# Performance work log

Measured on AMD Instinct MI355X. Metric: run time of the kernel, lower is better.

## Reference

```python
import jax, jax.numpy as jnp
import numpy as np

EPS = 1e-12

def _pdist(a, b):
    # a: [B,N,3], b: [B,M,3] -> [B,N,M] L2 distances (no huge [B,N,M,3] temp)
    sq = (jnp.sum(a * a, -1)[:, :, None] + jnp.sum(b * b, -1)[:, None, :]
          - 2.0 * jnp.einsum('bnd,bmd->bnm', a, b))
    return jnp.sqrt(jnp.maximum(sq, EPS))

def _loss_terms(skel_xyz, skel_radius, skel_nori, l3_xyz, shape_all):
    normal = shape_all[:, :, 3:6]
    shape_xyz = shape_all[:, :, :3]
    B, Ns, _ = skel_xyz.shape
    N = shape_xyz.shape[1]

    # --- loss_sample: 8 surface samples per sphere ---
    e = 0.57735027
    dirs = jnp.array([[e, e, e], [e, e, -e], [e, -e, e], [e, -e, -e],
                      [-e, e, e], [-e, e, -e], [-e, -e, e], [-e, -e, -e]],
                     dtype=skel_xyz.dtype)
    centers = jnp.repeat(skel_xyz, 8, axis=1)
    radii = jnp.repeat(skel_radius, 8, axis=1)
    sample_xyz = centers + radii * jnp.tile(dirs, (Ns, 1))[None]

    d_ss = _pdist(shape_xyz, sample_xyz)
    cd1 = jnp.sum(jnp.min(d_ss, axis=1)) / (Ns * 8)    # sample -> shape
    cd2 = jnp.sum(jnp.min(d_ss, axis=2)) / N           # shape -> sample
    loss_sample = cd1 + cd2

    # --- point2sphere / sphere2point ---
    d_sc = _pdist(shape_xyz, skel_xyz)                 # [B, N, Ns]
    sph = jnp.abs(d_sc - skel_radius[:, None, :, 0])
    loss_p2s = jnp.sum(jnp.min(sph, axis=2)) / N + jnp.sum(jnp.min(sph, axis=1)) / Ns

    loss_radius = -jnp.sum(skel_radius) / Ns

    # --- loss_normal: 30-NN of skel in shape, |dot(nori, shape normal)| ---
    d_ks = _pdist(skel_xyz, shape_xyz)                 # [B, Ns, N]
    idx30 = jax.lax.top_k(-d_ks, 30)[1]                # [B, Ns, 30]
    nn_nrm = jnp.take_along_axis(normal[:, None, :, :], idx30[..., None], axis=2)
    dots = jnp.einsum('bjd,bjkd->bjk', skel_nori, nn_nrm)
    loss_normal = jnp.sum(jnp.mean(jnp.abs(dots), axis=2)) / B

    # --- loss_skelenormal: points swept along nori, vs l3_xyz ---
    ks = (jnp.arange(30, dtype=skel_xyz.dtype) / 30.0)[None, :, None, None]
    combine = (skel_xyz[:, None] + skel_nori[:, None] * ks).reshape(B, 30 * Ns, 3)
    mind = jnp.min(_pdist(combine, l3_xyz), axis=2)
    loss_skn = 50.0 * jnp.sum(mind) / (B * Ns * 30)
    loss_skn = loss_skn + 500.0 * jnp.sum(jnp.var(mind, axis=1, ddof=1)) / B

    # --- loss_normaldist: exp barrier + hard penalty on |nori| ---
    nrm = jnp.sqrt(jnp.sum(skel_nori * skel_nori, -1) + EPS)
    loss_nd = jnp.sum(jnp.exp(-(nrm - 0.3)) + jnp.where(nrm < 0.25, 5.0, 0.0)) / (B * Ns)

    # --- loss_normalsmooth: 3-NN (incl. self) nori consistency ---
    idx3 = jax.lax.top_k(-_pdist(skel_xyz, skel_xyz), 3)[1]   # [B, Ns, 3]
    nn_nori = jnp.take_along_axis(skel_nori[:, None, :, :], idx3[..., None], axis=2)
    diff = skel_nori[:, :, None, :] - nn_nori
    loss_ns = jnp.sum(jnp.sqrt(jnp.sum(diff * diff, -1) + EPS)) / (B * Ns * 3)

    return loss_sample, loss_p2s, loss_radius, loss_normal, loss_skn, loss_nd, loss_ns

def setup_inputs() -> dict:
    key = jax.random.key(0)
    ks = jax.random.split(key, 9)
    B, N, Ns, M = 8, 4096, 256, 256
    return {
        'skel_xyz': jax.random.normal(ks[0], (B, Ns, 3), jnp.float32),
        'skel_radius': jax.random.uniform(ks[1], (B, Ns, 1), jnp.float32),
        'shape_cmb_features': jax.random.normal(ks[2], (B, Ns, 32), jnp.float32),
        'skel_nori': jax.random.normal(ks[3], (B, Ns, 3), jnp.float32),
        'weights': jax.random.uniform(ks[4], (B, Ns, 8), jnp.float32),
        'l3_xyz': jax.random.normal(ks[5], (B, M, 3), jnp.float32),
        'l3_normals': jax.random.normal(ks[6], (B, M, 3), jnp.float32),
        'shape_xyz': jax.random.normal(ks[7], (B, N, 6), jnp.float32),
        'A': jax.random.uniform(ks[8], (B, Ns, Ns), jnp.float32),
        'w0': 1, 'w1': 1, 'w2': 1, 'w3': 1, 'w4': 1, 'w5': 1, 'w6': 1,
    }

def reference(skel_xyz, skel_radius, shape_cmb_features, skel_nori, weights,
              l3_xyz, l3_normals, shape_xyz, A,
              w0, w1, w2, w3, w4, w5, w6):
    ls, lp, lr, ln, lskn, lnd, lns = _loss_terms(
        skel_xyz, skel_radius, skel_nori, l3_xyz, shape_xyz)
    # lap_reg=False -> loss_smooth = 0 (w3 term vanishes)
    return (w0 * ls + lp * w1 + lr * w2 + ln * w4 + lskn * w5
            + w6 * lnd + 0.1 * lns)
```

## Files before the change

kernel.cpp:

```cpp
#include <hip/hip_runtime.h>
#include <math.h>

#define EPS 1e-12f
#define EDIR 0.57735027f
#define M2E  -1.15470054f

#define NB 8
#define NS 256
#define NP 4096
#define NM 256

#define NBLK_MEGA 2048

#define OFF_SKO 0
#define OFF_C1O (OFF_SKO + 2048*4)
#define OFF_C2O (OFF_C1O + 2048)
#define OFF_P2O (OFF_C2O + 4096)
#define OFF_SKS (OFF_P2O + 4096)
#define OFF_SKQ (OFF_SKS + 960)

typedef float f4u __attribute__((ext_vector_type(4), aligned(4)));
typedef float f2u __attribute__((ext_vector_type(2), aligned(4)));

__device__ __forceinline__ unsigned umin2(unsigned a, unsigned b){ return a<b?a:b; }
__device__ __forceinline__ unsigned umax2(unsigned a, unsigned b){ return a>b?a:b; }

__device__ __forceinline__ float wave_min(float v){
#pragma unroll
  for (int o = 32; o; o >>= 1) v = fminf(v, __shfl_xor(v, o));
  return v;
}
__device__ __forceinline__ float wave_max(float v){
#pragma unroll
  for (int o = 32; o; o >>= 1) v = fmaxf(v, __shfl_xor(v, o));
  return v;
}
__device__ __forceinline__ float wave_sum(float v){
#pragma unroll
  for (int o = 32; o; o >>= 1) v += __shfl_xor(v, o);
  return v;
}
__device__ __forceinline__ unsigned wave_min_u(unsigned v){
#pragma unroll
  for (int o = 32; o; o >>= 1){ unsigned w = __shfl_xor(v, o); v = (w < v) ? w : v; }
  return v;
}
__device__ __forceinline__ unsigned wave_max_u(unsigned v){
#pragma unroll
  for (int o = 32; o; o >>= 1){ unsigned w = __shfl_xor(v, o); v = (w > v) ? w : v; }
  return v;
}
__device__ __forceinline__ unsigned long long wave_min_u64(unsigned long long v){
#pragma unroll
  for (int o = 32; o; o >>= 1){
    unsigned long long w = __shfl_xor(v, o);
    v = (w < v) ? w : v;
  }
  return v;
}

__global__ __launch_bounds__(256) void k_mega(const float* __restrict__ skel,
                                              const float* __restrict__ rad,
                                              const float* __restrict__ nori,
                                              const float* __restrict__ l3,
                                              const float* __restrict__ shape,
                                              float* __restrict__ ws){
  __shared__ float4 lsh[NM];
  int bid  = blockIdx.x;
  int tid  = threadIdx.x;
  int wid  = tid >> 6;
  int lane = tid & 63;

  if (wid == 0){
    int row = bid;
    int b = row >> 8;
    const float* sjp = skel + (size_t)row * 3;
    float cx = sjp[0], cy = sjp[1], cz = sjp[2];
    float rj = rad[row];
    float r2j = rj * rj;
    float m2re = M2E * rj;
    const float* njp = nori + (size_t)row * 3;
    float nx = njp[0], ny = njp[1], nz = njp[2];
    const float* shb = shape + (size_t)b * NP * 6;

    unsigned a0=~0u,a1=~0u,a2=~0u,a3=~0u,a4=~0u,a5=~0u;
    unsigned b0=~0u,b1=~0u,b2=~0u,b3=~0u,b4=~0u,b5=~0u;
    float dmoA = 3.4e38f, dmiA = -3.4e38f, dmoB = 3.4e38f, dmiB = -3.4e38f;
    float mn[8];
#pragma unroll
    for (int k = 0; k < 8; ++k) mn[k] = 3.4e38f;

#pragma unroll 2
    for (int s = 0; s < 32; ++s){
      int nA = s * 128 + lane;
      int nB = nA + 64;
      f4u qA = *(const f4u*)(shb + (size_t)nA * 6);
      f4u qB = *(const f4u*)(shb + (size_t)nB * 6);
      float dxA = qA.x - cx, dyA = qA.y - cy, dzA = qA.z - cz;
      float dxB = qB.x - cx, dyB = qB.y - cy, dzB = qB.z - cz;
      float dA = fmaf(dxA, dxA, fmaf(dyA, dyA, dzA * dzA));
      float dB = fmaf(dxB, dxB, fmaf(dyB, dyB, dzB * dzB));
      {
        float s1p = dxA + dyA, s2p = dxA - dyA;
        float ga = s1p + dzA, gb = s1p - dzA, gc = s2p + dzA, gd = s2p - dzA;
        mn[0] = fminf(mn[0], fmaf(m2re,  ga, dA));
        mn[1] = fminf(mn[1], fmaf(m2re,  gb, dA));
        mn[2] = fminf(mn[2], fmaf(m2re,  gc, dA));
        mn[3] = fminf(mn[3], fmaf(m2re,  gd, dA));
        mn[4] = fminf(mn[4], fmaf(m2re, -gd, dA));
        mn[5] = fminf(mn[5], fmaf(m2re, -gc, dA));
        mn[6] = fminf(mn[6], fmaf(m2re, -gb, dA));
        mn[7] = fminf(mn[7], fmaf(m2re, -ga, dA));
      }
      {
        float s1p = dxB + dyB, s2p = dxB - dyB;
        float ga = s1p + dzB, gb = s1p - dzB, gc = s2p + dzB, gd = s2p - dzB;
        mn[0] = fminf(mn[0], fmaf(m2re,  ga, dB));
        mn[1] = fminf(mn[1], fmaf(m2re,  gb, dB));
        mn[2] = fminf(mn[2], fmaf(m2re,  gc, dB));
        mn[3] = fminf(mn[3], fmaf(m2re,  gd, dB));
        mn[4] = fminf(mn[4], fmaf(m2re, -gd, dB));
        mn[5] = fminf(mn[5], fmaf(m2re, -gc, dB));
        mn[6] = fminf(mn[6], fmaf(m2re, -gb, dB));
        mn[7] = fminf(mn[7], fmaf(m2re, -ga, dB));
      }
      bool inA = dA < r2j;
      bool inB = dB < r2j;
      dmoA = fminf(dmoA, inA ? 3.4e38f : dA);
      dmiA = fmaxf(dmiA, inA ? dA : -3.4e38f);
      dmoB = fminf(dmoB, inB ? 3.4e38f : dB);
      dmiB = fmaxf(dmiB, inB ? dB : -3.4e38f);
      unsigned uA = (__float_as_uint(dA) & 0xFFFFF000u) | (unsigned)nA;
      unsigned uB = (__float_as_uint(dB) & 0xFFFFF000u) | (unsigned)nB;
      a5 = umin2(a5, uA);
      { unsigned p = umin2(a4, a5), q = umax2(a4, a5); a4 = p; a5 = q; }
      { unsigned p = umin2(a3, a4), q = umax2(a3, a4); a3 = p; a4 = q; }
      { unsigned p = umin2(a2, a3), q = umax2(a2, a3); a2 = p; a3 = q; }
      { unsigned p = umin2(a1, a2), q = umax2(a1, a2); a1 = p; a2 = q; }
      { unsigned p = umin2(a0, a1), q = umax2(a0, a1); a0 = p; a1 = q; }
      b5 = umin2(b5, uB);
      { unsigned p = umin2(b4, b5), q = umax2(b4, b5); b4 = p; b5 = q; }
      { unsigned p = umin2(b3, b4), q = umax2(b3, b4); b3 = p; b4 = q; }
      { unsigned p = umin2(b2, b3), q = umax2(b2, b3); b2 = p; b3 = q; }
      { unsigned p = umin2(b1, b2), q = umax2(b1, b2); b1 = p; b2 = q; }
      { unsigned p = umin2(b0, b1), q = umax2(b0, b1); b0 = p; b1 = q; }
    }
    {
      float v = 0.0f;
#pragma unroll
      for (int k = 0; k < 8; ++k){
        float m = wave_min(mn[k]);
        v += sqrtf(fmaxf(m + r2j, EPS));
      }
      if (lane == 0) ws[OFF_C1O + row] = v;
    }
    float dmin_out = wave_min(fminf(dmoA, dmoB));
    float dmax_in  = wave_max(fmaxf(dmiA, dmiB));
    float pmin = sqrtf(fmaxf(dmin_out, EPS)) - rj;
    float pin  = (dmax_in >= 0.0f) ? (rj - sqrtf(fmaxf(dmax_in, EPS))) : 3.4e38f;
    pmin = fminf(pmin, pin);

    unsigned lmin = umin2(a0, b0);
    unsigned lo = wave_min_u(lmin), hi = wave_max_u(lmin);
    while (lo < hi){
      unsigned mid = lo + ((hi - lo) >> 1);
      int c = __popcll(__ballot(a0 <= mid)) + __popcll(__ballot(a1 <= mid)) +
              __popcll(__ballot(a2 <= mid)) + __popcll(__ballot(a3 <= mid)) +
              __popcll(__ballot(a4 <= mid)) + __popcll(__ballot(a5 <= mid)) +
              __popcll(__ballot(b0 <= mid)) + __popcll(__ballot(b1 <= mid)) +
              __popcll(__ballot(b2 <= mid)) + __popcll(__ballot(b3 <= mid)) +
              __popcll(__ballot(b4 <= mid)) + __popcll(__ballot(b5 <= mid));
      if (c >= 30) hi = mid; else lo = mid + 1;
    }
    unsigned tau = hi;

    float dsum = 0.0f;
    {
      unsigned mm[12] = {a0,a1,a2,a3,a4,a5,b0,b1,b2,b3,b4,b5};
#pragma unroll
      for (int r = 0; r < 12; ++r){
        if (mm[r] <= tau){
          int idx = (int)(mm[r] & 0xFFFu);
          f4u qq = *(const f4u*)(shb + (size_t)idx * 6 + 2);
          dsum += fabsf(fmaf(nx, qq.y, fmaf(ny, qq.z, nz * qq.w)));
        }
      }
    }
    dsum = wave_sum(dsum);

    const float* skb = skel + (size_t)b * NS * 3;
    const float* nb  = nori + (size_t)b * NS * 3;
    unsigned u0=~0u,u1=~0u,u2=~0u; int i0=0,i1=0,i2=0;
#pragma unroll
    for (int it = 0; it < 4; ++it){
      int n2i = it * 64 + lane;
      f2u kxy = *(const f2u*)(skb + (size_t)n2i * 3);
      float kz = skb[(size_t)n2i * 3 + 2];
      float dx = kxy.x - cx, dy = kxy.y - cy, dz = kz - cz;
      unsigned u = __float_as_uint(fmaf(dx,dx,fmaf(dy,dy,dz*dz)));
      if (u < u2){ u2 = u; i2 = n2i; }
      if (u2 < u1){ unsigned t=u1;u1=u2;u2=t; int ti=i1;i1=i2;i2=ti; }
      if (u1 < u0){ unsigned t=u0;u0=u1;u1=t; int ti=i0;i0=i1;i1=ti; }
    }
    int cc = 0;
    float nssum = 0.0f;
#pragma unroll
    for (int r = 0; r < 3; ++r){
      unsigned hu = (cc==0)?u0:((cc==1)?u1:u2);
      int      hix= (cc==0)?i0:((cc==1)?i1:i2);
      unsigned long long pack = (((unsigned long long)hu) << 32) | (unsigned)hix;
      unsigned long long best = wave_min_u64(pack);
      if (pack == best) cc++;
      int idx = (int)(best & 0xffffffffull);
      if (lane == 0){
        float axn = nb[idx*3+0]-nx, ayn = nb[idx*3+1]-ny, azn = nb[idx*3+2]-nz;
        nssum += sqrtf(fmaf(axn,axn,fmaf(ayn,ayn,azn*azn)) + EPS);
      }
    }

    if (lane == 0){
      float nrm = sqrtf(nx*nx + ny*ny + nz*nz + EPS);
      float ndv = expf(0.3f - nrm) + ((nrm < 0.25f) ? 5.0f : 0.0f);
      float* sko = ws + OFF_SKO + (size_t)row * 4;
      sko[0] = pmin;
      sko[1] = dsum * (1.0f / 30.0f);
      sko[2] = nssum;
      sko[3] = ndv;
    }

  } else if (wid <= 2){
    int wv   = bid * 2 + (wid - 1);
    int row0 = wv * 8;
    int b    = row0 >> 12;
    float cx[8], cy[8], cz[8];
#pragma unroll
    for (int i = 0; i < 8; ++i){
      f4u qp = *(const f4u*)(shape + (size_t)(row0 + i) * 6);
      cx[i] = qp.x; cy[i] = qp.y; cz[i] = qp.z;
    }
    const float* skb = skel + (size_t)b * NS * 3;
    const float* rdb = rad + (size_t)b * NS;
    float mn[8], pm[8];
#pragma unroll
    for (int i = 0; i < 8; ++i){ mn[i] = 3.4e38f; pm[i] = 3.4e38f; }
#pragma unroll
    for (int it = 0; it < 4; ++it){
      int kidx = it * 64 + lane;
      f2u kxy = *(const f2u*)(skb + (size_t)kidx * 3);
      float kz = skb[(size_t)kidx * 3 + 2];
      float rr = rdb[kidx];
      float r2 = rr * rr;
      float c1 = M2E * rr;
#pragma unroll
      for (int i = 0; i < 8; ++i){
        float dx = cx[i] - kxy.x, dy = cy[i] - kxy.y, dz = cz[i] - kz;
        float q  = fmaf(dx, dx, fmaf(dy, dy, dz * dz));
        float s  = (fabsf(dx) + fabsf(dy)) + fabsf(dz);
        mn[i] = fminf(mn[i], fmaf(c1, s, q + r2));
        float d = sqrtf(fmaxf(q, EPS));
        pm[i] = fminf(pm[i], fabsf(d - rr));
      }
    }
    float cdv = 0.0f, pv = 0.0f;
#pragma unroll
    for (int i = 0; i < 8; ++i){
      float m = wave_min(mn[i]);
      cdv += sqrtf(fmaxf(m, EPS));
      pv  += wave_min(pm[i]);
    }
    if (lane == 0){
      ws[OFF_C2O + wv] = cdv;
      ws[OFF_P2O + wv] = pv;
    }

  } else {
    int q = bid;
    if (q >= 960) return;
    int b = q / 120;
    int w = q % 120;
    int t = w * 64 + lane;
    for (int i = lane; i < NM; i += 64){
      const float* lp = l3 + (size_t)(b * NM + i) * 3;
      float lx = lp[0], ly = lp[1], lz = lp[2];
      lsh[i] = make_float4(lx, ly, lz, fmaf(lx, lx, fmaf(ly, ly, lz * lz)));
    }
    int s = t >> 8;
    int j = t & 255;
    float ksf = (float)s * (1.0f / 30.0f);
    const float* sj = skel + (size_t)(b * NS + j) * 3;
    const float* nj = nori + (size_t)(b * NS + j) * 3;
    float px = fmaf(nj[0], ksf, sj[0]);
    float py = fmaf(nj[1], ksf, sj[1]);
    float pz = fmaf(nj[2], ksf, sj[2]);
    float ax = -2.0f * px, ay = -2.0f * py, az = -2.0f * pz;
    float pw = fmaf(px, px, fmaf(py, py, pz * pz));
    float mn = 3.4e38f;
#pragma unroll 8
    for (int qq = 0; qq < NM; ++qq){
      float4 L = lsh[qq];
      float t2 = fmaf(L.x, ax, fmaf(L.y, ay, fmaf(L.z, az, L.w)));
      mn = fminf(mn, t2);
    }
    float d = sqrtf(fmaxf(mn + pw, EPS));
    float s1 = wave_sum(d);
    float s2 = wave_sum(d * d);
    if (lane == 0){
      ws[OFF_SKS + q] = s1;
      ws[OFF_SKQ + q] = s2;
    }
  }
}

__global__ __launch_bounds__(1024) void k_final(const float* __restrict__ rad,
                                                const float* __restrict__ ws,
                                                const int* w0, const int* w1, const int* w2,
                                                const int* w4, const int* w5, const int* w6,
                                                float* __restrict__ out){
  __shared__ float red[8][16];
  __shared__ float sb1[960], sb2[960];
  __shared__ float bb1[8], bb2[8];
  int tid = threadIdx.x;
  int wid = tid >> 6, lane = tid & 63;

  float pp2sj = 0.0f, pnorm = 0.0f, pns = 0.0f, pnd = 0.0f;
  for (int q = tid; q < 2048; q += 1024){
    float4 s4 = *(const float4*)(ws + OFF_SKO + (size_t)q * 4);
    pp2sj += s4.x; pnorm += s4.y; pns += s4.z; pnd += s4.w;
  }
  float pc1 = 0.0f;
  for (int q = tid; q < 2048; q += 1024) pc1 += ws[OFF_C1O + q];
  float pc2 = 0.0f, pp2n = 0.0f;
  for (int q = tid; q < 4096; q += 1024){
    pc2  += ws[OFF_C2O + q];
    pp2n += ws[OFF_P2O + q];
  }
  float prad = 0.0f;
  for (int q = tid; q < NB * NS; q += 1024) prad += rad[q];

  if (tid < 960){ sb1[tid] = ws[OFF_SKS + tid]; sb2[tid] = ws[OFF_SKQ + tid]; }

  pp2sj = wave_sum(pp2sj); pnorm = wave_sum(pnorm);
  pns = wave_sum(pns);     pnd = wave_sum(pnd);
  pc1 = wave_sum(pc1);     pc2 = wave_sum(pc2);
  pp2n = wave_sum(pp2n);   prad = wave_sum(prad);
  if (lane == 0){
    red[0][wid] = pp2sj; red[1][wid] = pnorm; red[2][wid] = pns; red[3][wid] = pnd;
    red[4][wid] = pc1;   red[5][wid] = pc2;   red[6][wid] = pp2n; red[7][wid] = prad;
  }
  __syncthreads();
  if (tid < 8){
    float s1 = 0.0f, s2 = 0.0f;
    for (int i = 0; i < 120; ++i){ s1 += sb1[tid * 120 + i]; s2 += sb2[tid * 120 + i]; }
    bb1[tid] = s1; bb2[tid] = s2;
  }
  __syncthreads();
  if (tid == 0){
    float acc[8];
#pragma unroll
    for (int r = 0; r < 8; ++r){
      float v = 0.0f;
#pragma unroll
      for (int i = 0; i < 16; ++i) v += red[r][i];
      acc[r] = v;
    }
    float p2sj = acc[0], nrmt = acc[1], nst = acc[2], ndt = acc[3];
    float c1t = acc[4], c2t = acc[5], p2nt = acc[6], srad = acc[7];
    float ls = c1t * (1.0f/2048.0f) + c2t * (1.0f/4096.0f);
    float lp = p2nt * (1.0f/4096.0f) + p2sj * (1.0f/256.0f);
    float lr = -srad * (1.0f/256.0f);
    float ln = nrmt * (1.0f/8.0f);
    float smind = 0.0f, vsum = 0.0f;
    for (int b = 0; b < NB; ++b){
      float s1 = bb1[b], s2 = bb2[b];
      smind += s1;
      vsum  += (s2 - s1 * s1 * (1.0f/7680.0f)) * (1.0f/7679.0f);
    }
    float lskn = 50.0f * smind * (1.0f/(8.0f*7680.0f)) + 500.0f * vsum * (1.0f/8.0f);
    float lnd = ndt * (1.0f/2048.0f);
    float lns = nst * (1.0f/6144.0f);
    float o = (float)w0[0]*ls + (float)w1[0]*lp + (float)w2[0]*lr +
              (float)w4[0]*ln + (float)w5[0]*lskn + (float)w6[0]*lnd + 0.1f*lns;
    out[0] = o;
  }
}

extern "C" void kernel_launch(void* const* d_in, const int* in_sizes, int n_in,
                              void* d_out, int out_size, void* d_ws, size_t ws_size,
                              hipStream_t stream) {
  const float* skel  = (const float*)d_in[0];
  const float* rad   = (const float*)d_in[1];
  const float* nori  = (const float*)d_in[3];
  const float* l3    = (const float*)d_in[5];
  const float* shape = (const float*)d_in[7];
  const int* w0 = (const int*)d_in[9];
  const int* w1 = (const int*)d_in[10];
  const int* w2 = (const int*)d_in[11];
  const int* w4 = (const int*)d_in[13];
  const int* w5 = (const int*)d_in[14];
  const int* w6 = (const int*)d_in[15];
  float* ws  = (float*)d_ws;
  float* out = (float*)d_out;

  k_mega<<<dim3(NBLK_MEGA), dim3(256), 0, stream>>>(skel, rad, nori, l3, shape, ws);
  k_final<<<dim3(1), dim3(1024), 0, stream>>>(rad, ws, w0, w1, w2, w4, w5, w6, out);
}
```

Baseline: 51.12 us.

## Split per-skeleton shape scan across two waves and rebalance wave roles

The per-skeleton-row scan over all shape points was done by a single wave. It is now split so waves 0 and 1 each scan half of the points. Wave 1 passes its partial top-k keys and partial minima to wave 0 through LDS, and wave 0 merges them after a block barrier. The shape-to-sample work, formerly spread over waves 1 and 2, now runs on waves 2 and 3, and wave 3 also does the skeleton-normal sweep. The aim is to shorten the longest per-wave critical path. In exchange, the threshold bisection now counts over twice as many candidate keys, and the block adds a barrier plus LDS traffic.

```diff
diff --git a/kernel.cpp b/kernel.cpp
--- a/kernel.cpp
+++ b/kernel.cpp
@@ -57,6 +57,54 @@
     v = (w < v) ? w : v;
   }
   return v;
+}
+
+__device__ __forceinline__ void cd2_role(int wv, const float* __restrict__ skel,
+                                         const float* __restrict__ rad,
+                                         const float* __restrict__ shape,
+                                         float* __restrict__ ws, int lane){
+  int row0 = wv * 8;
+  int b    = row0 >> 12;
+  float cx[8], cy[8], cz[8];
+#pragma unroll
+  for (int i = 0; i < 8; ++i){
+    f4u qp = *(const f4u*)(shape + (size_t)(row0 + i) * 6);
+    cx[i] = qp.x; cy[i] = qp.y; cz[i] = qp.z;
+  }
+  const float* skb = skel + (size_t)b * NS * 3;
+  const float* rdb = rad + (size_t)b * NS;
+  float mn[8], pm[8];
+#pragma unroll
+  for (int i = 0; i < 8; ++i){ mn[i] = 3.4e38f; pm[i] = 3.4e38f; }
+#pragma unroll
+  for (int it = 0; it < 4; ++it){
+    int kidx = it * 64 + lane;
+    f2u kxy = *(const f2u*)(skb + (size_t)kidx * 3);
+    float kz = skb[(size_t)kidx * 3 + 2];
+    float rr = rdb[kidx];
+    float r2 = rr * rr;
+    float c1 = M2E * rr;
+#pragma unroll
+    for (int i = 0; i < 8; ++i){
+      float dx = cx[i] - kxy.x, dy = cy[i] - kxy.y, dz = cz[i] - kz;
+      float q  = fmaf(dx, dx, fmaf(dy, dy, dz * dz));
+      float s  = (fabsf(dx) + fabsf(dy)) + fabsf(dz);
+      mn[i] = fminf(mn[i], fmaf(c1, s, q + r2));
+      float d = sqrtf(fmaxf(q, EPS));
+      pm[i] = fminf(pm[i], fabsf(d - rr));
+    }
+  }
+  float cdv = 0.0f, pv = 0.0f;
+#pragma unroll
+  for (int i = 0; i < 8; ++i){
+    float m = wave_min(mn[i]);
+    cdv += sqrtf(fmaxf(m, EPS));
+    pv  += wave_min(pm[i]);
+  }
+  if (lane == 0){
+    ws[OFF_C2O + wv] = cdv;
+    ws[OFF_P2O + wv] = pv;
+  }
 }
 
 __global__ __launch_bounds__(256) void k_mega(const float* __restrict__ skel,
@@ -66,12 +114,14 @@
                                               const float* __restrict__ shape,
                                               float* __restrict__ ws){
   __shared__ float4 lsh[NM];
+  __shared__ unsigned wkeys[64 * 13];
+  __shared__ float wpart[10];
   int bid  = blockIdx.x;
   int tid  = threadIdx.x;
   int wid  = tid >> 6;
   int lane = tid & 63;
 
-  if (wid == 0){
+  if (wid <= 1){
     int row = bid;
     int b = row >> 8;
     const float* sjp = skel + (size_t)row * 3;
@@ -79,9 +129,8 @@
     float rj = rad[row];
     float r2j = rj * rj;
     float m2re = M2E * rj;
-    const float* njp = nori + (size_t)row * 3;
-    float nx = njp[0], ny = njp[1], nz = njp[2];
     const float* shb = shape + (size_t)b * NP * 6;
+    int s0 = wid * 16;
 
     unsigned a0=~0u,a1=~0u,a2=~0u,a3=~0u,a4=~0u,a5=~0u;
     unsigned b0=~0u,b1=~0u,b2=~0u,b3=~0u,b4=~0u,b5=~0u;
@@ -91,7 +140,8 @@
     for (int k = 0; k < 8; ++k) mn[k] = 3.4e38f;
 
 #pragma unroll 2
-    for (int s = 0; s < 32; ++s){
+    for (int si = 0; si < 16; ++si){
+      int s = s0 + si;
       int nA = s * 128 + lane;
       int nB = nA + 64;
       f4u qA = *(const f4u*)(shb + (size_t)nA * 6);
@@ -145,22 +195,47 @@
       { unsigned p = umin2(b1, b2), q = umax2(b1, b2); b1 = p; b2 = q; }
       { unsigned p = umin2(b0, b1), q = umax2(b0, b1); b0 = p; b1 = q; }
     }
+    float mnr[8];
+#pragma unroll
+    for (int k = 0; k < 8; ++k) mnr[k] = wave_min(mn[k]);
+    float dmo = wave_min(fminf(dmoA, dmoB));
+    float dmi = wave_max(fmaxf(dmiA, dmiB));
+
+    if (wid == 1){
+      unsigned* wk = wkeys + lane * 13;
+      wk[0]=a0; wk[1]=a1; wk[2]=a2; wk[3]=a3; wk[4]=a4; wk[5]=a5;
+      wk[6]=b0; wk[7]=b1; wk[8]=b2; wk[9]=b3; wk[10]=b4; wk[11]=b5;
+      if (lane == 0){
+#pragma unroll
+        for (int k = 0; k < 8; ++k) wpart[k] = mnr[k];
+        wpart[8] = dmo; wpart[9] = dmi;
+      }
+      __syncthreads();
+      return;
+    }
+    __syncthreads();
+    unsigned c0,c1,c2,c3,c4,c5,c6,c7,c8,c9,c10,c11;
+    {
+      const unsigned* wk = wkeys + lane * 13;
+      c0=wk[0]; c1=wk[1]; c2=wk[2]; c3=wk[3]; c4=wk[4]; c5=wk[5];
+      c6=wk[6]; c7=wk[7]; c8=wk[8]; c9=wk[9]; c10=wk[10]; c11=wk[11];
+    }
     {
       float v = 0.0f;
 #pragma unroll
       for (int k = 0; k < 8; ++k){
-        float m = wave_min(mn[k]);
+        float m = fminf(mnr[k], wpart[k]);
         v += sqrtf(fmaxf(m + r2j, EPS));
       }
       if (lane == 0) ws[OFF_C1O + row] = v;
     }
-    float dmin_out = wave_min(fminf(dmoA, dmoB));
-    float dmax_in  = wave_max(fmaxf(dmiA, dmiB));
+    float dmin_out = fminf(dmo, wpart[8]);
+    float dmax_in  = fmaxf(dmi, wpart[9]);
     float pmin = sqrtf(fmaxf(dmin_out, EPS)) - rj;
     float pin  = (dmax_in >= 0.0f) ? (rj - sqrtf(fmaxf(dmax_in, EPS))) : 3.4e38f;
     pmin = fminf(pmin, pin);
 
-    unsigned lmin = umin2(a0, b0);
+    unsigned lmin = umin2(umin2(a0, b0), umin2(c0, c6));
     unsigned lo = wave_min_u(lmin), hi = wave_max_u(lmin);
     while (lo < hi){
       unsigned mid = lo + ((hi - lo) >> 1);
@@ -169,16 +244,25 @@
               __popcll(__ballot(a4 <= mid)) + __popcll(__ballot(a5 <= mid)) +
               __popcll(__ballot(b0 <= mid)) + __popcll(__ballot(b1 <= mid)) +
               __popcll(__ballot(b2 <= mid)) + __popcll(__ballot(b3 <= mid)) +
-              __popcll(__ballot(b4 <= mid)) + __popcll(__ballot(b5 <= mid));
+              __popcll(__ballot(b4 <= mid)) + __popcll(__ballot(b5 <= mid)) +
+              __popcll(__ballot(c0 <= mid)) + __popcll(__ballot(c1 <= mid)) +
+              __popcll(__ballot(c2 <= mid)) + __popcll(__ballot(c3 <= mid)) +
+              __popcll(__ballot(c4 <= mid)) + __popcll(__ballot(c5 <= mid)) +
+              __popcll(__ballot(c6 <= mid)) + __popcll(__ballot(c7 <= mid)) +
+              __popcll(__ballot(c8 <= mid)) + __popcll(__ballot(c9 <= mid)) +
+              __popcll(__ballot(c10 <= mid)) + __popcll(__ballot(c11 <= mid));
       if (c >= 30) hi = mid; else lo = mid + 1;
     }
     unsigned tau = hi;
 
+    const float* njp = nori + (size_t)row * 3;
+    float nx = njp[0], ny = njp[1], nz = njp[2];
     float dsum = 0.0f;
     {
-      unsigned mm[12] = {a0,a1,a2,a3,a4,a5,b0,b1,b2,b3,b4,b5};
-#pragma unroll
-      for (int r = 0; r < 12; ++r){
+      unsigned mm[24] = {a0,a1,a2,a3,a4,a5,b0,b1,b2,b3,b4,b5,
+                         c0,c1,c2,c3,c4,c5,c6,c7,c8,c9,c10,c11};
+#pragma unroll
+      for (int r = 0; r < 24; ++r){
         if (mm[r] <= tau){
           int idx = (int)(mm[r] & 0xFFFu);
           f4u qq = *(const f4u*)(shb + (size_t)idx * 6 + 2);
@@ -227,55 +311,18 @@
       sko[2] = nssum;
       sko[3] = ndv;
     }
-
-  } else if (wid <= 2){
-    int wv   = bid * 2 + (wid - 1);
-    int row0 = wv * 8;
-    int b    = row0 >> 12;
-    float cx[8], cy[8], cz[8];
-#pragma unroll
-    for (int i = 0; i < 8; ++i){
-      f4u qp = *(const f4u*)(shape + (size_t)(row0 + i) * 6);
-      cx[i] = qp.x; cy[i] = qp.y; cz[i] = qp.z;
-    }
-    const float* skb = skel + (size_t)b * NS * 3;
-    const float* rdb = rad + (size_t)b * NS;
-    float mn[8], pm[8];
-#pragma unroll
-    for (int i = 0; i < 8; ++i){ mn[i] = 3.4e38f; pm[i] = 3.4e38f; }
-#pragma unroll
-    for (int it = 0; it < 4; ++it){
-      int kidx = it * 64 + lane;
-      f2u kxy = *(const f2u*)(skb + (size_t)kidx * 3);
-      float kz = skb[(size_t)kidx * 3 + 2];
-      float rr = rdb[kidx];
-      float r2 = rr * rr;
-      float c1 = M2E * rr;
-#pragma unroll
-      for (int i = 0; i < 8; ++i){
-        float dx = cx[i] - kxy.x, dy = cy[i] - kxy.y, dz = cz[i] - kz;
-        float q  = fmaf(dx, dx, fmaf(dy, dy, dz * dz));
-        float s  = (fabsf(dx) + fabsf(dy)) + fabsf(dz);
-        mn[i] = fminf(mn[i], fmaf(c1, s, q + r2));
-        float d = sqrtf(fmaxf(q, EPS));
-        pm[i] = fminf(pm[i], fabsf(d - rr));
-      }
-    }
-    float cdv = 0.0f, pv = 0.0f;
-#pragma unroll
-    for (int i = 0; i < 8; ++i){
-      float m = wave_min(mn[i]);
-      cdv += sqrtf(fmaxf(m, EPS));
-      pv  += wave_min(pm[i]);
-    }
-    if (lane == 0){
-      ws[OFF_C2O + wv] = cdv;
-      ws[OFF_P2O + wv] = pv;
-    }
-
-  } else {
+    return;
+  }
+
+  if (wid == 2){
+    cd2_role(bid, skel, rad, shape, ws, lane);
+    __syncthreads();
+    return;
+  }
+
+  cd2_role(2048 + bid, skel, rad, shape, ws, lane);
+  if (bid < 960){
     int q = bid;
-    if (q >= 960) return;
     int b = q / 120;
     int w = q % 120;
     int t = w * 64 + lane;
@@ -294,14 +341,14 @@
     float pz = fmaf(nj[2], ksf, sj[2]);
     float ax = -2.0f * px, ay = -2.0f * py, az = -2.0f * pz;
     float pw = fmaf(px, px, fmaf(py, py, pz * pz));
-    float mn = 3.4e38f;
+    float mnv = 3.4e38f;
 #pragma unroll 8
     for (int qq = 0; qq < NM; ++qq){
       float4 L = lsh[qq];
       float t2 = fmaf(L.x, ax, fmaf(L.y, ay, fmaf(L.z, az, L.w)));
-      mn = fminf(mn, t2);
-    }
-    float d = sqrtf(fmaxf(mn + pw, EPS));
+      mnv = fminf(mnv, t2);
+    }
+    float d = sqrtf(fmaxf(mnv + pw, EPS));
     float s1 = wave_sum(d);
     float s2 = wave_sum(d * d);
     if (lane == 0){
@@ -309,6 +356,7 @@
       ws[OFF_SKQ + q] = s2;
     }
   }
+  __syncthreads();
 }
 
 __global__ __launch_bounds__(1024) void k_final(const float* __restrict__ rad,
```

Result: slower. 53.58 us (+4.8%).
